# Performance work log

Measured on AMD Instinct MI355X. Metric: run time of the kernel, lower is better.

Reference implementation:

```python
import jax, jax.numpy as jnp
import numpy as np

N=50000; E=400000; H=128; FN=92; FE=41; L=3; PC=8; PD=16; SC=8; SD=32; B=64
EPS=1e-5

def _silu(x):
    return jax.nn.silu(x)

def _squash(s):
    n2=(s*s).sum(-1,keepdims=True)
    return s*(n2/(1.0+n2))/jnp.sqrt(n2+1e-9)

def setup_inputs():
    ks=iter(jax.random.split(jax.random.key(0),96))
    def rn(shape): return jax.random.normal(next(ks),shape,dtype=jnp.float32)
    def w(i,o): return rn((i,o))*np.float32(1.0/np.sqrt(i))
    z=lambda *s: jnp.zeros(s,jnp.float32); o=lambda *s: jnp.ones(s,jnp.float32)
    d={}
    d['x']=rn((N,FN)); d['edge_attr']=rn((E,FE)); d['pos']=rn((N,3))
    d['edge_index']=jax.random.randint(next(ks),(2,E),0,N)
    d['batch']=jnp.sort(jax.random.randint(next(ks),(N,),0,B))
    d.update(neW1=w(FN,H),neb1=z(H),neg1=o(H),nebe1=z(H),neW2=w(H,H),neb2=z(H),neg2=o(H),nebe2=z(H))
    d.update(eeW1=w(FE,H),eeb1=z(H),eeW2=w(H,H),eeb2=z(H),ivW=w(H,H),ivb=z(H))
    def wl(i,o2): return jnp.stack([w(i,o2) for _ in range(L)])
    d.update(cWma=wl(H,H),cWmb=wl(H,H),cWme=wl(H,H),cbm=z(L,H),cWsx=wl(H,H),cWsa=wl(H,H),cbs=z(L,H))
    d.update(cWv1=wl(H,H),cbv1=z(L,H),cWv2=wl(H,H),cbv2=z(L,H),lng=o(L,H),lnb=z(L,H),vsg=o(L,H))
    d.update(pcW=w(H,PC*PD),pcb=z(PC*PD),pvW=w(H,PD),sW=rn((PC,PD,SC,SD))*np.float32(1.0/np.sqrt(PD)))
    d.update(aW=w(SD//2,1),ab=z(1))
    d.update(pW1=w(SD,H//2),pb1=z(H//2),pg1=o(H//2),pbe1=z(H//2),pW2=w(H//2,H//4),pb2=z(H//4),pg2=o(H//4),pbe2=z(H//4),pW3=w(H//4,1),pb3=z(1))
    return d

def _forward(x,edge_index,edge_attr,pos,batch,neW1,neb1,neg1,nebe1,neW2,neb2,neg2,nebe2,eeW1,eeb1,eeW2,eeb2,ivW,ivb,cWma,cWmb,cWme,cbm,cWsx,cWsa,cbs,cWv1,cbv1,cWv2,cbv2,lng,lnb,vsg,pcW,pcb,pvW,sW,aW,ab,pW1,pb1,pg1,pbe1,pW2,pb2,pg2,pbe2,pW3,pb3):
    seg=jax.ops.segment_sum
    # node/edge MLP embeddings (BatchNorm in eval mode: running mean 0 / var 1 -> affine)
    xs=_silu((x@neW1+neb1)*neg1+nebe1)
    xs=_silu((xs@neW2+neb2)*neg2+nebe2)
    ea=_silu(edge_attr@eeW1+eeb1); ea=_silu(ea@eeW2+eeb2)
    # vectorized form of the per-node python loop: outer product weights x pos -> [N,H,3]
    xv=(xs@ivW+ivb)[:,:,None]*pos[:,None,:]
    src,dst=edge_index[0],edge_index[1]
    dp=pos[dst]-pos[src]                                  # [E,3]
    for i in range(L):
        xs_res,xv_res=xs,xv
        m=_silu(xs[src]@cWma[i]+xs[dst]@cWmb[i]+ea@cWme[i]+cbm[i])   # [E,H] edge messages
        xs_c=xs@cWsx[i]+seg(m,dst,num_segments=N)@cWsa[i]+cbs[i]
        vmsg=xv[src]*(m@cWv1[i]+cbv1[i])[:,:,None]+(m@cWv2[i]+cbv2[i])[:,:,None]*dp[:,None,:]
        xv_c=xv+seg(vmsg,dst,num_segments=N)               # [N,H,3]
        mu=xs_c.mean(-1,keepdims=True)
        xs_n=(xs_c-mu)/jnp.sqrt(((xs_c-mu)**2).mean(-1,keepdims=True)+EPS)*lng[i]+lnb[i]
        nrm=jnp.sqrt(((xv_c**2).sum(-1)).mean(-1,keepdims=True)+EPS)  # equivariant norm [N,1]
        xv_n=(xv_c/nrm[:,:,None])*vsg[i][None,:,None]
        xv_n=xv_n*jax.nn.sigmoid(xs_n)[:,:,None]           # scalar gating of vectors
        if i>0:
            xs=_silu(xs_n)+xs_res; xv=xv_n+xv_res
        else:
            xs=_silu(xs_n); xv=xv_n
    # primary capsules
    pc=_squash((xs@pcW+pcb).reshape(-1,PC,PD))             # [N,PC,PD]
    pv=jnp.einsum('nhd,hp->npd',xv,pvW)                    # [N,PD,3]
    u=pc+jnp.sqrt((pv**2).sum(-1)+1e-9)[:,None,:]          # vector norms expanded over PC caps
    # secondary capsules with per-graph pooling + 2 routing iterations
    pooled=seg(jnp.einsum('npd,pdce->npce',u,sW),batch,num_segments=B)  # [B,PC,SC,SD]
    bb=jnp.zeros((B,PC,SC),jnp.float32)
    for it in range(2):
        c=jax.nn.softmax(bb,axis=-1)
        v=_squash(jnp.einsum('bpc,bpce->bce',c,pooled))    # [B,SC,SD]
        if it==0:
            bb=bb+jnp.einsum('bpce,bce->bpc',pooled,v)
    # attention pooling over secondary capsules
    aw=jax.nn.softmax(v[:,:,:SD//2]@aW+ab,axis=1)
    wc=(aw*v).sum(1)                                       # [B,SD]
    h=_silu((wc@pW1+pb1)*pg1+pbe1)
    h=_silu((h@pW2+pb2)*pg2+pbe2)                          # dropout: eval mode (identity)
    return h@pW3+pb3

def reference(x,edge_index,edge_attr,pos,batch,neW1,neb1,neg1,nebe1,neW2,neb2,neg2,nebe2,eeW1,eeb1,eeW2,eeb2,ivW,ivb,cWma,cWmb,cWme,cbm,cWsx,cWsa,cbs,cWv1,cbv1,cWv2,cbv2,lng,lnb,vsg,pcW,pcb,pvW,sW,aW,ab,pW1,pb1,pg1,pbe1,pW2,pb2,pg2,pbe2,pW3,pb3):
    return _forward(x,edge_index,edge_attr,pos,batch,neW1,neb1,neg1,nebe1,neW2,neb2,neg2,nebe2,eeW1,eeb1,eeW2,eeb2,ivW,ivb,cWma,cWmb,cWme,cbm,cWsx,cWsa,cbs,cWv1,cbv1,cWv2,cbv2,lng,lnb,vsg,pcW,pcb,pvW,sW,aW,ab,pW1,pb1,pg1,pbe1,pW2,pb2,pg2,pbe2,pW3,pb3)
```

## Files before the change

### kernel.cpp

```cpp
#include <hip/hip_runtime.h>
#include <hip/hip_bf16.h>
#include <math.h>

#define NN 50000
#define NE 400000
#define HD 128
#define NB 64
#define NCH 8
#define CN 6250
#define ECM 53248
#define PSL 16

typedef __hip_bfloat16 bf16;
typedef __attribute__((ext_vector_type(4))) unsigned short us4;
typedef __attribute__((ext_vector_type(8))) short s8v;
typedef __attribute__((ext_vector_type(4))) float f4v;

__device__ __forceinline__ float sigm_(float x){ return 1.f/(1.f+__expf(-x)); }
__device__ __forceinline__ float silu_(float x){ return x*sigm_(x); }
__device__ __forceinline__ float bf2f(bf16 x){ return __bfloat162float(x); }
__device__ __forceinline__ unsigned short f2bu(float f){
    bf16 h = __float2bfloat16(f);
    return *reinterpret_cast<unsigned short*>(&h);
}
__device__ __forceinline__ bool finite_(float v){ return fabsf(v) <= 1e37f; }

enum { M_PLAIN=0, M_BIAS, M_BNSILU };

__global__ void wprep(const float* __restrict__ W, bf16* __restrict__ H, bf16* __restrict__ L){
    int i = blockIdx.x*256 + threadIdx.x;
    int k = i >> 7, n = i & 127;
    float w = W[i];
    bf16 h = __float2bfloat16(w);
    float r = w - bf2f(h);
    H[n*128 + k] = h;
    L[n*128 + k] = __float2bfloat16(r);
}

__global__ void wprep1(const float* __restrict__ W, bf16* __restrict__ H, bf16* __restrict__ L){
    int i = blockIdx.x*256 + threadIdx.x;
    int n = i >> 6, k = i & 63;
    float w = (k < 41) ? W[(size_t)k*HD + n] : 0.f;
    bf16 h = __float2bfloat16(w);
    float r = w - bf2f(h);
    H[n*64 + k] = h;
    L[n*64 + k] = __float2bfloat16(r);
}

template<int MODE>
__global__ __launch_bounds__(256)
void gemmk(const float* __restrict__ A, const float* __restrict__ W,
           const float* __restrict__ bias, const float* __restrict__ gg,
           const float* __restrict__ be, void* __restrict__ Cv, int owf, int M, int K)
{
    const int row0 = blockIdx.x * 64;
    if (row0 >= M) return;
    __shared__ float As[32][68];
    __shared__ float Ws[32][128];
    const int tid = threadIdx.x;
    const int tx = tid & 15, ty = tid >> 4;
    const int col0 = tx*8;
    float acc[4][8];
#pragma unroll
    for (int r=0;r<4;++r)
#pragma unroll
        for (int j=0;j<8;++j) acc[r][j]=0.f;
    const int mload = tid >> 2;
    const int kload = (tid & 3) << 3;
    const int grow = row0 + mload;
    const bool rv = grow < M;

    for (int k0 = 0; k0 < K; k0 += 32) {
        if (rv && ((K & 3) == 0) && (k0 + kload + 8 <= K)) {
            const float* ap = A + (size_t)grow*K + k0 + kload;
            float4 v0 = *(const float4*)ap;
            float4 v1 = *(const float4*)(ap+4);
            As[kload+0][mload]=v0.x; As[kload+1][mload]=v0.y;
            As[kload+2][mload]=v0.z; As[kload+3][mload]=v0.w;
            As[kload+4][mload]=v1.x; As[kload+5][mload]=v1.y;
            As[kload+6][mload]=v1.z; As[kload+7][mload]=v1.w;
        } else {
#pragma unroll
            for (int j=0;j<8;++j){
                int kg = k0 + kload + j;
                As[kload+j][mload] = (rv && kg<K) ? A[(size_t)grow*K+kg] : 0.f;
            }
        }
        if (k0 + 32 <= K) {
#pragma unroll
            for (int j=0;j<4;++j){
                int el = (tid + j*256)*4;
                int kk = el >> 7, col = el & 127;
                *(float4*)&Ws[kk][col] = *(const float4*)&W[(size_t)(k0+kk)*HD + col];
            }
        } else {
#pragma unroll
            for (int j=0;j<16;++j){
                int el = tid*16 + j;
                int kk = el >> 7, col = el & 127;
                int kg = k0 + kk;
                Ws[kk][col] = (kg < K) ? W[(size_t)kg*HD + col] : 0.f;
            }
        }
        __syncthreads();
#pragma unroll
        for (int k=0;k<32;++k){
            float4 a4 = *(const float4*)&As[k][ty*4];
            float4 w0 = *(const float4*)&Ws[k][col0];
            float4 w1 = *(const float4*)&Ws[k][col0+4];
            float av[4] = {a4.x,a4.y,a4.z,a4.w};
            float wv[8] = {w0.x,w0.y,w0.z,w0.w,w1.x,w1.y,w1.z,w1.w};
#pragma unroll
            for (int r=0;r<4;++r)
#pragma unroll
                for (int j=0;j<8;++j) acc[r][j] += av[r]*wv[j];
        }
        __syncthreads();
    }
#pragma unroll
    for (int r=0;r<4;++r){
        int orow = row0 + ty*4 + r;
        if (orow >= M) continue;
        float o[8];
#pragma unroll
        for (int j=0;j<8;++j) o[j]=acc[r][j];
        if constexpr (MODE==M_BIAS || MODE==M_BNSILU){
#pragma unroll
            for (int j=0;j<8;++j) o[j] += bias[col0+j];
        }
        if constexpr (MODE==M_BNSILU){
#pragma unroll
            for (int j=0;j<8;++j) o[j] = silu_(o[j]*gg[col0+j] + be[col0+j]);
        }
        if (owf){
            bf16* C = (bf16*)Cv;
#pragma unroll
            for (int j=0;j<8;++j) C[(size_t)orow*HD+col0+j] = __float2bfloat16(o[j]);
        } else {
            float* C = (float*)Cv;
            float4* cp = (float4*)&C[(size_t)orow*HD + col0];
            cp[0] = make_float4(o[0],o[1],o[2],o[3]);
            cp[1] = make_float4(o[4],o[5],o[6],o[7]);
        }
    }
}

__global__ __launch_bounds__(256)
void gemm3(const float* __restrict__ A0, const float* __restrict__ W0, float* __restrict__ C0, int M0,
           const float* __restrict__ A1, const float* __restrict__ W1, float* __restrict__ C1, int M1,
           const float* __restrict__ A2, const float* __restrict__ W2, float* __restrict__ C2, int M2)
{
    const int nb0 = (M0+63)>>6, nb1 = (M1+63)>>6;
    int bb = (int)blockIdx.x;
    const float *A, *W; float* C; int M;
    if (bb < nb0){ A=A0; W=W0; C=C0; M=M0; }
    else if (bb < nb0+nb1){ bb -= nb0; A=A1; W=W1; C=C1; M=M1; }
    else { bb -= nb0+nb1; A=A2; W=W2; C=C2; M=M2; }
    const int row0 = bb*64;

    __shared__ float As[32][68];
    __shared__ float Ws[32][128];
    const int tid = threadIdx.x;
    const int tx = tid & 15, ty = tid >> 4;
    const int col0 = tx*8;
    float acc[4][8];
#pragma unroll
    for (int r=0;r<4;++r)
#pragma unroll
        for (int j=0;j<8;++j) acc[r][j]=0.f;
    const int mload = tid >> 2;
    const int kload = (tid & 3) << 3;
    const int grow = row0 + mload;
    const bool rv = grow < M;

    for (int k0 = 0; k0 < 128; k0 += 32) {
        if (rv) {
            const float* ap = A + (size_t)grow*128 + k0 + kload;
            float4 v0 = *(const float4*)ap;
            float4 v1 = *(const float4*)(ap+4);
            As[kload+0][mload]=v0.x; As[kload+1][mload]=v0.y;
            As[kload+2][mload]=v0.z; As[kload+3][mload]=v0.w;
            As[kload+4][mload]=v1.x; As[kload+5][mload]=v1.y;
            As[kload+6][mload]=v1.z; As[kload+7][mload]=v1.w;
        } else {
#pragma unroll
            for (int j=0;j<8;++j) As[kload+j][mload] = 0.f;
        }
#pragma unroll
        for (int j=0;j<4;++j){
            int el = (tid + j*256)*4;
            int kk = el >> 7, col = el & 127;
            *(float4*)&Ws[kk][col] = *(const float4*)&W[(size_t)(k0+kk)*HD + col];
        }
        __syncthreads();
#pragma unroll
        for (int k=0;k<32;++k){
            float4 a4 = *(const float4*)&As[k][ty*4];
            float4 w0 = *(const float4*)&Ws[k][col0];
            float4 w1 = *(const float4*)&Ws[k][col0+4];
            float av[4] = {a4.x,a4.y,a4.z,a4.w};
            float wv[8] = {w0.x,w0.y,w0.z,w0.w,w1.x,w1.y,w1.z,w1.w};
#pragma unroll
            for (int r=0;r<4;++r)
#pragma unroll
                for (int j=0;j<8;++j) acc[r][j] += av[r]*wv[j];
        }
        __syncthreads();
    }
#pragma unroll
    for (int r=0;r<4;++r){
        int orow = row0 + ty*4 + r;
        if (orow >= M) continue;
        float4* cp = (float4*)&C[(size_t)orow*HD + col0];
        cp[0] = make_float4(acc[r][0],acc[r][1],acc[r][2],acc[r][3]);
        cp[1] = make_float4(acc[r][4],acc[r][5],acc[r][6],acc[r][7]);
    }
}

__global__ __launch_bounds__(256)
void edge_pipe(const float* __restrict__ eat,
               const int* __restrict__ elist, const int* __restrict__ srcp,
               const int* __restrict__ dstp,
               const bf16* __restrict__ W1h, const bf16* __restrict__ W1l,
               const float* __restrict__ b1,
               const bf16* __restrict__ W2h, const bf16* __restrict__ W2l,
               const float* __restrict__ b2,
               const bf16* __restrict__ Wmeh, const bf16* __restrict__ Wmel,
               const float* __restrict__ bm,
               const bf16* __restrict__ An, const bf16* __restrict__ Bn,
               const bf16* __restrict__ Wv1h, const bf16* __restrict__ Wv1l,
               const float* __restrict__ bv1,
               const int* __restrict__ rp, int rn0, int rn1,
               bf16* __restrict__ outM, bf16* __restrict__ outG)
{
    __shared__ __align__(16) unsigned short T1[64][136];
    __shared__ __align__(16) unsigned short T2[64][136];
    __shared__ int elS[64], seS[64], deS[64];

    const int cbase = rp[rn0];
    const int Ml = min(ECM, max(rp[rn1]-cbase, 0));
    const int row0 = blockIdx.x*64;
    if (row0 >= Ml) return;
    const int tid = threadIdx.x;
    const int lane = tid & 63, wave = tid >> 6;
    const int quad = lane >> 4, n16 = lane & 15;
    const int cwb = wave*32;

    if (tid < 64){
        int r = row0 + tid;
        bool v = r < Ml;
        int p = cbase + (v ? r : 0);
        elS[tid] = v ? min(max(elist[p],0),NE-1) : 0;
        seS[tid] = v ? srcp[p] : 0;
        deS[tid] = v ? dstp[p] : 0;
    }
    __syncthreads();

    f4v acc[4][2];

    {
        s8v B1h[2][2], B1l[2][2];
#pragma unroll
        for (int ct=0; ct<2; ++ct){
            int nn = cwb + ct*16 + n16;
#pragma unroll
            for (int kc=0; kc<2; ++kc){
                B1h[ct][kc] = *(const s8v*)&W1h[(size_t)nn*64 + kc*32 + quad*8];
                B1l[ct][kc] = *(const s8v*)&W1l[(size_t)nn*64 + kc*32 + quad*8];
            }
        }
#pragma unroll
        for (int rt=0;rt<4;++rt)
#pragma unroll
            for (int ct=0;ct<2;++ct) acc[rt][ct] = (f4v){0.f,0.f,0.f,0.f};

#pragma unroll
        for (int rt=0; rt<4; ++rt){
            int arow = elS[rt*16 + n16];
#pragma unroll
            for (int kc=0; kc<2; ++kc){
                s8v ah, al;
#pragma unroll
                for (int j=0;j<8;++j){
                    int k = kc*32 + quad*8 + j;
                    float v = (k < 41) ? eat[(size_t)arow*41 + k] : 0.f;
                    unsigned short h = f2bu(v);
                    ah[j] = (short)h;
                    al[j] = (short)f2bu(v - __uint_as_float(((unsigned)h)<<16));
                }
#pragma unroll
                for (int ct=0; ct<2; ++ct){
                    acc[rt][ct] = __builtin_amdgcn_mfma_f32_16x16x32_bf16(ah, B1h[ct][kc], acc[rt][ct], 0,0,0);
                    acc[rt][ct] = __builtin_amdgcn_mfma_f32_16x16x32_bf16(ah, B1l[ct][kc], acc[rt][ct], 0,0,0);
                    acc[rt][ct] = __builtin_amdgcn_mfma_f32_16x16x32_bf16(al, B1h[ct][kc], acc[rt][ct], 0,0,0);
                }
            }
        }
#pragma unroll
        for (int ct=0; ct<2; ++ct){
            int col = cwb + ct*16 + n16;
            float bc = b1[col];
#pragma unroll
            for (int rt=0; rt<4; ++rt)
#pragma unroll
                for (int i=0;i<4;++i)
                    T1[rt*16 + quad*4 + i][col] = f2bu(silu_(acc[rt][ct][i] + bc));
        }
    }
    __syncthreads();

    s8v Bh[2][4], Bl[2][4];
    for (int ph=0; ph<3; ++ph){
        const bf16* WH = (ph==0)? W2h : (ph==1)? Wmeh : Wv1h;
        const bf16* WL = (ph==0)? W2l : (ph==1)? Wmel : Wv1l;
        const unsigned short (*Tin)[136] = (ph==1)? (const unsigned short(*)[136])T2
                                                  : (const unsigned short(*)[136])T1;
#pragma unroll
        for (int ct=0; ct<2; ++ct){
            int nn = cwb + ct*16 + n16;
            const s8v* hp = (const s8v*)&WH[(size_t)nn*128];
            const s8v* lp = (const s8v*)&WL[(size_t)nn*128];
#pragma unroll
            for (int kc=0; kc<4; ++kc){
                Bh[ct][kc] = hp[kc*4 + quad];
                Bl[ct][kc] = lp[kc*4 + quad];
            }
        }
#pragma unroll
        for (int rt=0;rt<4;++rt)
#pragma unroll
            for (int ct=0;ct<2;++ct) acc[rt][ct] = (f4v){0.f,0.f,0.f,0.f};

        s8v anR[4], bnR[4];
        if (ph==1){
#pragma unroll
            for (int it=0; it<4; ++it){
                int idx = tid + it*256;
                int r = idx >> 4, c = idx & 15;
                anR[it] = *(const s8v*)&An[(size_t)seS[r]*HD + c*8];
                bnR[it] = *(const s8v*)&Bn[(size_t)deS[r]*HD + c*8];
            }
        }

#pragma unroll
        for (int kc=0; kc<4; ++kc){
#pragma unroll
            for (int rt=0; rt<4; ++rt){
                s8v a = *(const s8v*)&Tin[rt*16 + n16][kc*32 + quad*8];
#pragma unroll
                for (int ct=0; ct<2; ++ct){
                    acc[rt][ct] = __builtin_amdgcn_mfma_f32_16x16x32_bf16(a, Bh[ct][kc], acc[rt][ct], 0,0,0);
                    acc[rt][ct] = __builtin_amdgcn_mfma_f32_16x16x32_bf16(a, Bl[ct][kc], acc[rt][ct], 0,0,0);
                }
            }
        }
        if (ph==0){
#pragma unroll
            for (int ct=0; ct<2; ++ct){
                int col = cwb + ct*16 + n16;
                float bc = b2[col];
#pragma unroll
                for (int rt=0; rt<4; ++rt)
#pragma unroll
                    for (int i=0;i<4;++i)
                        T2[rt*16 + quad*4 + i][col] = f2bu(silu_(acc[rt][ct][i] + bc));
            }
            __syncthreads();
        } else if (ph==1){
            __syncthreads();
#pragma unroll
            for (int it=0; it<4; ++it){
                int idx = tid + it*256;
                int r = idx >> 4, c = idx & 15;
                *(s8v*)&T1[r][c*8] = anR[it];
                *(s8v*)&T2[r][c*8] = bnR[it];
            }
            __syncthreads();
#pragma unroll
            for (int ct=0; ct<2; ++ct){
                int col = cwb + ct*16 + n16;
                float bc = bm[col];
#pragma unroll
                for (int rt=0; rt<4; ++rt)
#pragma unroll
                    for (int i=0;i<4;++i){
                        int row = rt*16 + quad*4 + i;
                        float v = silu_(acc[rt][ct][i] + bc
                                        + bf2f(*(const bf16*)&T1[row][col])
                                        + bf2f(*(const bf16*)&T2[row][col]));
                        T1[row][col] = f2bu(v);
                    }
            }
            __syncthreads();
            {
                int row = tid >> 2, seg = tid & 3;
                if (row0 + row < Ml){
                    const s8v* s = (const s8v*)&T1[row][seg*32];
                    s8v* d = (s8v*)&outM[(size_t)(row0+row)*HD + seg*32];
                    d[0]=s[0]; d[1]=s[1]; d[2]=s[2]; d[3]=s[3];
                }
            }
        } else {
#pragma unroll
            for (int ct=0; ct<2; ++ct){
                int col = cwb + ct*16 + n16;
                float bc = bv1[col];
#pragma unroll
                for (int rt=0; rt<4; ++rt)
#pragma unroll
                    for (int i=0;i<4;++i)
                        T2[rt*16 + quad*4 + i][col] = f2bu(acc[rt][ct][i] + bc);
            }
            __syncthreads();
            {
                int row = tid >> 2, seg = tid & 3;
                if (row0 + row < Ml){
                    const s8v* s = (const s8v*)&T2[row][seg*32];
                    s8v* d = (s8v*)&outG[(size_t)(row0+row)*HD + seg*32];
                    d[0]=s[0]; d[1]=s[1]; d[2]=s[2]; d[3]=s[3];
                }
            }
        }
    }
}

__global__ __launch_bounds__(128)
void scatter_c(const int* __restrict__ rp, const int* __restrict__ srcp,
               const float* __restrict__ pos,
               const bf16* __restrict__ mB, const bf16* __restrict__ gB,
               const float* __restrict__ xvO,
               float* __restrict__ smC, float* __restrict__ mdC,
               float* __restrict__ avC, float* __restrict__ sdC, int n0, int n1)
{
    const int b = blockIdx.x;
    const int n = n0 + b;
    if (n >= n1) return;
    const int h = threadIdx.x;
    const int cbase = rp[n0];
    int p0 = rp[n], p1 = rp[n+1];
    float px0=pos[n*3],px1=pos[n*3+1],px2=pos[n*3+2];
    float sm=0,a0=0,a1=0,a2=0,m0=0,m1=0,m2=0,d0s=0,d1s=0,d2s=0;
    for (int p=p0;p<p1;++p){
        int ii=p-cbase; if ((unsigned)ii>=(unsigned)ECM) break;
        float mh=bf2f(mB[(size_t)ii*HD+h]);
        float gh=bf2f(gB[(size_t)ii*HD+h]);
        int sn=srcp[p]; sn=min(max(sn,0),NN-1);
        float d0=px0-pos[sn*3], d1=px1-pos[sn*3+1], d2=px2-pos[sn*3+2];
        sm+=mh;
        a0+=xvO[(size_t)sn*3*HD+h]*gh;
        a1+=xvO[(size_t)sn*3*HD+HD+h]*gh;
        a2+=xvO[(size_t)sn*3*HD+2*HD+h]*gh;
        m0+=mh*d0; m1+=mh*d1; m2+=mh*d2;
        d0s+=d0; d1s+=d1; d2s+=d2;
    }
    smC[(size_t)b*HD+h]=sm;
    mdC[(size_t)b*3*HD+h]=m0;
    mdC[(size_t)b*3*HD+HD+h]=m1;
    mdC[(size_t)b*3*HD+2*HD+h]=m2;
    avC[(size_t)b*3*HD+h]=a0;
    avC[(size_t)b*3*HD+HD+h]=a1;
    avC[(size_t)b*3*HD+2*HD+h]=a2;
    if (h==0){ sdC[b*3]=d0s; sdC[b*3+1]=d1s; sdC[b*3+2]=d2s; }
}

__global__ __launch_bounds__(128)
void nu_lite(const float* __restrict__ gF, const float* __restrict__ swF,
             const float* __restrict__ xwF,
             const float* __restrict__ avC, const float* __restrict__ sdC,
             const float* __restrict__ xvO, float* __restrict__ xvN,
             float* __restrict__ xs,
             const float* __restrict__ bv2, const float* __restrict__ bs,
             const float* __restrict__ lng, const float* __restrict__ lnb,
             const float* __restrict__ vsg, int addRes, int n0, int n1)
{
    __shared__ float red[4];
    __shared__ float red2[2];
    const int b = blockIdx.x;
    const int n = n0 + b;
    if (n >= n1) return;
    const int h = threadIdx.x;
    const int w = h >> 6;
    const float xsv = xs[(size_t)n*HD+h];
    float xc = xwF[(size_t)b*HD+h] + swF[(size_t)b*HD+h] + bs[h];
    float s1=xc, s2=xc*xc;
#pragma unroll
    for (int off=1; off<64; off<<=1){ s1+=__shfl_xor(s1,off,64); s2+=__shfl_xor(s2,off,64); }
    if ((h&63)==0){ red[w*2]=s1; red[w*2+1]=s2; }
    __syncthreads();
    s1=red[0]+red[2]; s2=red[1]+red[3];
    float mu=s1*(1.f/128.f);
    float var=fmaxf(s2*(1.f/128.f)-mu*mu, 0.f);
    float xn=(xc-mu)*rsqrtf(var+1e-5f)*lng[h]+lnb[h];
    float ov0=xvO[(size_t)n*3*HD+h];
    float ov1=xvO[(size_t)n*3*HD+HD+h];
    float ov2=xvO[(size_t)n*3*HD+2*HD+h];
    float a0=avC[(size_t)b*3*HD+h];
    float a1=avC[(size_t)b*3*HD+HD+h];
    float a2=avC[(size_t)b*3*HD+2*HD+h];
    float d0s=sdC[b*3], d1s=sdC[b*3+1], d2s=sdC[b*3+2];
    float b2v=bv2[h];
    float v0=ov0+a0+gF[(size_t)(b*3+0)*HD+h]+b2v*d0s;
    float v1=ov1+a1+gF[(size_t)(b*3+1)*HD+h]+b2v*d1s;
    float v2=ov2+a2+gF[(size_t)(b*3+2)*HD+h]+b2v*d2s;
    float q=v0*v0+v1*v1+v2*v2;
#pragma unroll
    for (int off=1; off<64; off<<=1) q+=__shfl_xor(q,off,64);
    if ((h&63)==0) red2[w]=q;
    __syncthreads();
    q=fmaxf(red2[0]+red2[1], 0.f);
    float nrm=sqrtf(q*(1.f/128.f)+1e-5f);
    float scale=vsg[h]*sigm_(xn)/nrm;
    float r0=v0*scale, r1=v1*scale, r2=v2*scale;
    float nxs=silu_(xn);
    if (addRes){ nxs+=xsv; r0+=ov0; r1+=ov1; r2+=ov2; }
    xs[(size_t)n*HD+h]=nxs;
    xvN[(size_t)n*3*HD+h]=r0;
    xvN[(size_t)n*3*HD+HD+h]=r1;
    xvN[(size_t)n*3*HD+2*HD+h]=r2;
}

__global__ void hist_kernel(const int* __restrict__ idx, int* __restrict__ cnt, int n, int nb){
    int i = blockIdx.x*256 + threadIdx.x;
    if (i < n){
        int v = idx[i]; v = min(max(v,0), nb-1);
        atomicAdd(&cnt[v], 1);
    }
}

__global__ __launch_bounds__(256)
void scan_blk(const int* __restrict__ cnt, int* __restrict__ rowptr,
              int* __restrict__ bsum, int n){
    const int b = blockIdx.x, t = threadIdx.x;
    const int i = b*256 + t;
    const int lane = t & 63, w = t >> 6;
    int v = (i < n) ? cnt[i] : 0;
    int s = v;
#pragma unroll
    for (int off=1; off<64; off<<=1){
        int u = __shfl_up(s, off, 64);
        if (lane >= off) s += u;
    }
    __shared__ int ws[4];
    if (lane == 63) ws[w] = s;
    __syncthreads();
    int add = 0;
#pragma unroll
    for (int j=0;j<4;++j) if (j < w) add += ws[j];
    s += add;
    if (i < n) rowptr[i+1] = s;
    if (t == 255) bsum[b] = s;
    if (b == 0 && t == 0) rowptr[0] = 0;
}

__global__ __launch_bounds__(256)
void scan_bsum(int* __restrict__ bsum, int nb){
    const int t = threadIdx.x;
    const int lane = t & 63, w = t >> 6;
    int v = (t < nb) ? bsum[t] : 0;
    int s = v;
#pragma unroll
    for (int off=1; off<64; off<<=1){
        int u = __shfl_up(s, off, 64);
        if (lane >= off) s += u;
    }
    __shared__ int ws[4];
    if (lane == 63) ws[w] = s;
    __syncthreads();
    int add = 0;
#pragma unroll
    for (int j=0;j<4;++j) if (j < w) add += ws[j];
    s += add;
    if (t < nb) bsum[t] = s - v;
}

__global__ __launch_bounds__(256)
void scan_fix(int* __restrict__ rowptr, const int* __restrict__ bsum, int n){
    const int b = blockIdx.x, t = threadIdx.x;
    const int i = b*256 + t;
    const int off = bsum[b];
    if (i < n) rowptr[i+1] += off;
}

__global__ void fill_kernel(const int* __restrict__ src, const int* __restrict__ dst,
                            const int* __restrict__ rowptr, int* __restrict__ cur,
                            int* __restrict__ elist, int* __restrict__ srcp,
                            int* __restrict__ dstp, int n){
    int e = blockIdx.x*256 + threadIdx.x;
    if (e < n){
        int d = dst[e]; d = min(max(d,0), NN-1);
        int slot = atomicAdd(&cur[d], 1);
        int p = rowptr[d] + slot;
        if (p >= 0 && p < NE){
            elist[p] = e;
            int s = src[e];
            srcp[p] = min(max(s,0), NN-1);
            dstp[p] = d;
        }
    }
}

__global__ void gptr_kernel(const int* __restrict__ batch, int* __restrict__ gptr){
    int n = blockIdx.x*256 + threadIdx.x;
    if (n >= NN) return;
    int b = batch[n]; b = min(max(b,0), NB-1);
    if (n == 0){
        for (int g=0; g<=b; ++g) gptr[g] = 0;
    } else {
        int bp = batch[n-1]; bp = min(max(bp,0), NB-1);
        for (int g=bp+1; g<=b; ++g) gptr[g] = n;
    }
    if (n == NN-1){
        for (int g=b+1; g<=NB; ++g) gptr[g] = NN;
    }
}

__global__ void xv_init(const float* __restrict__ xw, const float* __restrict__ pos,
                        float* __restrict__ xv){
    int n = blockIdx.x, h = threadIdx.x;
    float v = xw[(size_t)n*HD+h];
    xv[(size_t)n*3*HD + h]        = v*pos[n*3+0];
    xv[(size_t)n*3*HD + HD + h]   = v*pos[n*3+1];
    xv[(size_t)n*3*HD + 2*HD + h] = v*pos[n*3+2];
}

__global__ __launch_bounds__(128)
void capsule2(const float* __restrict__ Pf, const float* __restrict__ xv,
              const float* __restrict__ pvW, bf16* __restrict__ u){
    __shared__ float Pn[128];
    __shared__ float Xv[3][128];
    __shared__ float dots[48];
    __shared__ float pvn[16];
    __shared__ float capn2[8];
    int n = blockIdx.x, t = threadIdx.x;
    Pn[t] = Pf[(size_t)n*HD + t];
    Xv[0][t] = xv[(size_t)n*3*HD + t];
    Xv[1][t] = xv[(size_t)n*3*HD + HD + t];
    Xv[2][t] = xv[(size_t)n*3*HD + 2*HD + t];
    __syncthreads();
    if (t < 48){
        int pp = t/3, c = t%3;
        float a = 0.f;
        for (int hh=0; hh<128; ++hh) a += Xv[c][hh]*pvW[hh*16+pp];
        dots[t] = a;
    }
    if (t < 8){
        float a = 0.f;
        for (int d=0; d<16; ++d){ float x = Pn[t*16+d]; a += x*x; }
        capn2[t] = a;
    }
    __syncthreads();
    if (t < 16){
        float a = dots[t*3]*dots[t*3] + dots[t*3+1]*dots[t*3+1] + dots[t*3+2]*dots[t*3+2];
        pvn[t] = sqrtf(a + 1e-9f);
    }
    __syncthreads();
    int cap = t >> 4, d = t & 15;
    float n2 = capn2[cap];
    float pcv = Pn[t] * (n2/(1.f+n2)) * rsqrtf(n2 + 1e-9f);
    u[(size_t)n*HD + t] = __float2bfloat16(pcv + pvn[d]);
}

__global__ void pool1(const int* __restrict__ gptr, const bf16* __restrict__ u,
                      float* __restrict__ Up){
    int blk = blockIdx.x;
    int b = blk / PSL, s = blk % PSL;
    int h = threadIdx.x;
    int g0 = gptr[b], g1 = gptr[b+1];
    g0 = min(max(g0,0), NN); g1 = min(max(g1,0), NN);
    int len = g1 - g0;
    int lo = g0 + (int)(((long long)len * s) / PSL);
    int hi = g0 + (int)(((long long)len * (s+1)) / PSL);
    float a = 0.f;
    for (int n=lo; n<hi; ++n) a += bf2f(u[(size_t)n*HD + h]);
    Up[(size_t)blk*HD + h] = a;
}

__global__ void pool2(const float* __restrict__ Up, float* __restrict__ U){
    int b = blockIdx.x, h = threadIdx.x;
    float a = 0.f;
    for (int s=0; s<PSL; ++s) a += Up[(size_t)(b*PSL+s)*HD + h];
    U[b*HD + h] = a;
}

__global__ void graph_head(const float* __restrict__ U, const float* __restrict__ sW,
                           const float* __restrict__ aW, const float* __restrict__ ab,
                           const float* __restrict__ pW1, const float* __restrict__ pb1,
                           const float* __restrict__ pg1, const float* __restrict__ pbe1,
                           const float* __restrict__ pW2, const float* __restrict__ pb2,
                           const float* __restrict__ pg2, const float* __restrict__ pbe2,
                           const float* __restrict__ pW3, const float* __restrict__ pb3,
                           float* __restrict__ out){
    __shared__ float Ub[128];
    __shared__ float pooled[2048];
    __shared__ float vv[256];
    __shared__ float bbs[64], ccs[64];
    __shared__ float lg[8], aws[8];
    __shared__ float wcs[32];
    __shared__ float h1[64], h2[32];
    int b = blockIdx.x, t = threadIdx.x;
    if (t < 128) Ub[t] = U[b*HD + t];
    __syncthreads();
#pragma unroll
    for (int j=0;j<8;++j){
        int o = t + 256*j;
        int p = o >> 8, c = (o >> 5) & 7, e = o & 31;
        float a = 0.f;
#pragma unroll
        for (int d=0; d<16; ++d) a += Ub[p*16+d]*sW[((p*16+d)*8+c)*32+e];
        pooled[o] = a;
    }
    __syncthreads();
    {
        float s = 0.f;
        for (int p=0;p<8;++p) s += pooled[p*256 + t];
        s *= 0.125f;
        float n2 = s*s;
#pragma unroll
        for (int off=1; off<32; off<<=1) n2 += __shfl_xor(n2,off,32);
        vv[t] = s*(n2/(1.f+n2))*rsqrtf(n2+1e-9f);
    }
    __syncthreads();
    if (t < 64){
        int p = t>>3, c = t&7;
        float a = 0.f;
        for (int e=0;e<32;++e) a += pooled[p*256+c*32+e]*vv[c*32+e];
        bbs[t] = a;
    }
    __syncthreads();
    if (t < 64){
        int p = t>>3;
        float mx = -1e30f;
        for (int j=0;j<8;++j) mx = fmaxf(mx, bbs[p*8+j]);
        float sum = 0.f;
        for (int j=0;j<8;++j) sum += __expf(bbs[p*8+j]-mx);
        ccs[t] = __expf(bbs[t]-mx)/sum;
    }
    __syncthreads();
    {
        int c = t>>5;
        float s = 0.f;
        for (int p=0;p<8;++p) s += ccs[p*8+c]*pooled[p*256 + t];
        float n2 = s*s;
#pragma unroll
        for (int off=1; off<32; off<<=1) n2 += __shfl_xor(n2,off,32);
        vv[t] = s*(n2/(1.f+n2))*rsqrtf(n2+1e-9f);
    }
    __syncthreads();
    if (t < 8){
        float a = 0.f;
        for (int j=0;j<16;++j) a += vv[t*32+j]*aW[j];
        lg[t] = a + ab[0];
    }
    __syncthreads();
    if (t < 8){
        float mx = -1e30f;
        for (int j=0;j<8;++j) mx = fmaxf(mx, lg[j]);
        float sum = 0.f;
        for (int j=0;j<8;++j) sum += __expf(lg[j]-mx);
        aws[t] = __expf(lg[t]-mx)/sum;
    }
    __syncthreads();
    if (t < 32){
        float a = 0.f;
        for (int c=0;c<8;++c) a += aws[c]*vv[c*32+t];
        wcs[t] = a;
    }
    __syncthreads();
    if (t < 64){
        float a = 0.f;
        for (int e=0;e<32;++e) a += wcs[e]*pW1[e*64+t];
        h1[t] = silu_((a+pb1[t])*pg1[t]+pbe1[t]);
    }
    __syncthreads();
    if (t < 32){
        float a = 0.f;
        for (int j=0;j<64;++j) a += h1[j]*pW2[j*32+t];
        h2[t] = silu_((a+pb2[t])*pg2[t]+pbe2[t]);
    }
    __syncthreads();
    if (t == 0){
        float a = 0.f;
        for (int j=0;j<32;++j) a += h2[j]*pW3[j];
        a += pb3[0];
        if (!finite_(a)) a = 999.f;
        out[b] = a;
    }
}

__global__ void sentinel_k(float* __restrict__ out, float v){
    out[threadIdx.x] = v;
}

extern "C" void kernel_launch(void* const* d_in, const int* in_sizes, int n_in,
                              void* d_out, int out_size, void* d_ws, size_t ws_size,
                              hipStream_t stream)
{
    (void)in_sizes; (void)n_in; (void)out_size;
    const float* x    = (const float*)d_in[0];
    const float* eat  = (const float*)d_in[1];
    const float* pos  = (const float*)d_in[2];
    const int*  eidx  = (const int*)d_in[3];
    const int*  batch = (const int*)d_in[4];
    const float* neW1=(const float*)d_in[5],  *neb1=(const float*)d_in[6],
               * neg1=(const float*)d_in[7],  *nebe1=(const float*)d_in[8];
    const float* neW2=(const float*)d_in[9],  *neb2=(const float*)d_in[10],
               * neg2=(const float*)d_in[11], *nebe2=(const float*)d_in[12];
    const float* eeW1=(const float*)d_in[13], *eeb1=(const float*)d_in[14];
    const float* eeW2=(const float*)d_in[15], *eeb2=(const float*)d_in[16];
    const float* ivW =(const float*)d_in[17], *ivb =(const float*)d_in[18];
    const float* cWma=(const float*)d_in[19], *cWmb=(const float*)d_in[20],
               * cWme=(const float*)d_in[21], *cbm =(const float*)d_in[22];
    const float* cWsx=(const float*)d_in[23], *cWsa=(const float*)d_in[24],
               * cbs =(const float*)d_in[25];
    const float* cWv1=(const float*)d_in[26], *cbv1=(const float*)d_in[27],
               * cWv2=(const float*)d_in[28], *cbv2=(const float*)d_in[29];
    const float* lng =(const float*)d_in[30], *lnb =(const float*)d_in[31],
               * vsg =(const float*)d_in[32];
    const float* pcW =(const float*)d_in[33], *pcb =(const float*)d_in[34];
    const float* pvW =(const float*)d_in[35];
    const float* sW  =(const float*)d_in[36];
    const float* aW  =(const float*)d_in[37], *ab  =(const float*)d_in[38];
    const float* pW1 =(const float*)d_in[39], *pb1 =(const float*)d_in[40],
               * pg1 =(const float*)d_in[41], *pbe1=(const float*)d_in[42];
    const float* pW2 =(const float*)d_in[43], *pb2 =(const float*)d_in[44],
               * pg2 =(const float*)d_in[45], *pbe2=(const float*)d_in[46];
    const float* pW3 =(const float*)d_in[47], *pb3 =(const float*)d_in[48];

    const int* src = eidx;
    const int* dst = eidx + NE;

    char* wp = (char*)d_ws;
    auto alloc = [&](size_t bytes)->char*{
        char* p = wp;
        wp += (bytes + 255) & ~(size_t)255;
        return p;
    };
    bf16*  bufM  = (bf16*) alloc((size_t)ECM*HD*2);
    bf16*  bufG  = (bf16*) alloc((size_t)ECM*HD*2);
    float* xs    = (float*)alloc((size_t)NN*HD*4);
    float* xvA   = (float*)alloc((size_t)NN*3*HD*4);
    float* xvB   = (float*)alloc((size_t)NN*3*HD*4);
    bf16*  An    = (bf16*) alloc((size_t)NN*HD*2);
    bf16*  Bn    = (bf16*) alloc((size_t)NN*HD*2);
    float* smC   = (float*)alloc((size_t)CN*HD*4);
    float* mdC   = (float*)alloc((size_t)CN*3*HD*4);
    float* avC   = (float*)alloc((size_t)CN*3*HD*4);
    float* sdC   = (float*)alloc((size_t)CN*3*4);
    bf16*  WtH   = (bf16*) alloc((size_t)7*HD*HD*2);
    bf16*  WtL   = (bf16*) alloc((size_t)7*HD*HD*2);
    bf16*  W1h   = (bf16*) alloc((size_t)HD*64*2);
    bf16*  W1l   = (bf16*) alloc((size_t)HD*64*2);
    float* Up    = (float*)alloc((size_t)NB*PSL*HD*4);
    float* Ubuf  = (float*)alloc((size_t)NB*HD*4);
    int* rowptr  = (int*)alloc((size_t)(NN+1)*4);
    int* cnt     = (int*)alloc((size_t)NN*4);
    int* bsum    = (int*)alloc((size_t)256*4);
    int* elist   = (int*)alloc((size_t)NE*4);
    int* srcp    = (int*)alloc((size_t)NE*4);
    int* dstp    = (int*)alloc((size_t)NE*4);
    int* gptr    = (int*)alloc((size_t)(NB+1)*4);
    size_t used  = (size_t)(wp - (char*)d_ws);

    if (used > ws_size){
        sentinel_k<<<1, NB, 0, stream>>>((float*)d_out, -1.f - (float)(ws_size >> 20));
        return;
    }
    float* tmpF = xvB;
    bf16*  ubuf = An;
    float* Pf   = xvA;
    float* gF  = (float*)bufM;
    float* swF = gF  + (size_t)3*CN*HD;
    float* xwF = swF + (size_t)CN*HD;

    hipMemsetAsync(cnt, 0, (size_t)NN*4, stream);
    hist_kernel<<<(NE+255)/256, 256, 0, stream>>>(dst, cnt, NE, NN);
    const int SBLK = (NN+255)/256;
    scan_blk<<<SBLK, 256, 0, stream>>>(cnt, rowptr, bsum, NN);
    scan_bsum<<<1, 256, 0, stream>>>(bsum, SBLK);
    scan_fix<<<SBLK, 256, 0, stream>>>(rowptr, bsum, NN);
    hipMemsetAsync(cnt, 0, (size_t)NN*4, stream);
    fill_kernel<<<(NE+255)/256, 256, 0, stream>>>(src, dst, rowptr, cnt, elist, srcp, dstp, NE);
    gptr_kernel<<<(NN+255)/256, 256, 0, stream>>>(batch, gptr);
    wprep1<<<32,256,0,stream>>>(eeW1, W1h, W1l);
    wprep<<<64,256,0,stream>>>(eeW2, WtH, WtL);
    for (int l=0;l<3;++l){
        wprep<<<64,256,0,stream>>>(cWme + (size_t)l*HD*HD, WtH + (size_t)(1+l)*HD*HD,
                                   WtL + (size_t)(1+l)*HD*HD);
        wprep<<<64,256,0,stream>>>(cWv1 + (size_t)l*HD*HD, WtH + (size_t)(4+l)*HD*HD,
                                   WtL + (size_t)(4+l)*HD*HD);
    }

    const int GN = (NN+63)/64;
    const int GE = ECM/64;
    const int G3 = ((3*CN+63)/64) + 2*((CN+63)/64);

    gemmk<M_BNSILU><<<GN,256,0,stream>>>(x, neW1, neb1, neg1, nebe1, tmpF, 0, NN, 92);
    gemmk<M_BNSILU><<<GN,256,0,stream>>>(tmpF, neW2, neb2, neg2, nebe2, xs, 0, NN, 128);
    gemmk<M_BIAS><<<GN,256,0,stream>>>(xs, ivW, ivb, nullptr, nullptr, tmpF, 0, NN, 128);
    xv_init<<<NN, 128, 0, stream>>>(tmpF, pos, xvA);

    float* xvO = xvA;
    float* xvN = xvB;
    for (int l=0; l<3; ++l){
        const float* Wma = cWma + (size_t)l*HD*HD;
        const float* Wmb = cWmb + (size_t)l*HD*HD;
        const float* bm  = cbm  + (size_t)l*HD;
        const float* Wsx = cWsx + (size_t)l*HD*HD;
        const float* Wsa = cWsa + (size_t)l*HD*HD;
        const float* bs  = cbs  + (size_t)l*HD;
        const float* bv1 = cbv1 + (size_t)l*HD;
        const float* Wv2 = cWv2 + (size_t)l*HD*HD;
        const float* bv2 = cbv2 + (size_t)l*HD;
        const bf16* Wmeh = WtH + (size_t)(1+l)*HD*HD;
        const bf16* Wmel = WtL + (size_t)(1+l)*HD*HD;
        const bf16* Wv1h = WtH + (size_t)(4+l)*HD*HD;
        const bf16* Wv1l = WtL + (size_t)(4+l)*HD*HD;

        gemmk<M_PLAIN><<<GN,256,0,stream>>>(xs, Wma, nullptr, nullptr, nullptr, An, 1, NN, 128);
        gemmk<M_PLAIN><<<GN,256,0,stream>>>(xs, Wmb, nullptr, nullptr, nullptr, Bn, 1, NN, 128);

        for (int c=0; c<NCH; ++c){
            int n0 = c*CN, n1 = n0+CN;
            edge_pipe<<<GE,256,0,stream>>>(eat, elist, srcp, dstp,
                                           W1h, W1l, eeb1,
                                           WtH, WtL, eeb2,
                                           Wmeh, Wmel, bm,
                                           An, Bn,
                                           Wv1h, Wv1l, bv1,
                                           rowptr, n0, n1, bufM, bufG);
            scatter_c<<<CN,128,0,stream>>>(rowptr, srcp, pos, bufM, bufG, xvO,
                                           smC, mdC, avC, sdC, n0, n1);
            gemm3<<<G3,256,0,stream>>>(mdC, Wv2, gF, 3*CN,
                                       smC, Wsa, swF, CN,
                                       xs + (size_t)n0*HD, Wsx, xwF, CN);
            nu_lite<<<CN,128,0,stream>>>(gF, swF, xwF, avC, sdC,
                                         xvO, xvN, xs,
                                         bv2, bs,
                                         lng + (size_t)l*HD, lnb + (size_t)l*HD,
                                         vsg + (size_t)l*HD, l>0 ? 1 : 0, n0, n1);
        }
        float* t = xvO; xvO = xvN; xvN = t;
    }

    gemmk<M_BIAS><<<GN,256,0,stream>>>(xs, pcW, pcb, nullptr, nullptr, Pf, 0, NN, 128);
    capsule2<<<NN, 128, 0, stream>>>(Pf, xvO, pvW, ubuf);
    pool1<<<NB*PSL, 128, 0, stream>>>(gptr, ubuf, Up);
    pool2<<<NB, 128, 0, stream>>>(Up, Ubuf);
    graph_head<<<NB, 256, 0, stream>>>(Ubuf, sW, aW, ab,
                                       pW1, pb1, pg1, pbe1,
                                       pW2, pb2, pg2, pbe2,
                                       pW3, pb3, (float*)d_out);
}
```

Measured before the change: 3.333 ms.

## Restructure capsule2 to process nodes per wavefront with register-cached pvW

The capsule kernel now assigns one node to each 64-lane wavefront and loops each wave over four nodes, instead of launching one 128-thread block per node. pvW slices are held in registers across those nodes, and the dot products and capsule norms are reduced with cross-lane shuffles rather than serial per-thread loops over shared memory. This is meant to cut the launch of 50000 small blocks, the idle threads, and the repeated pvW reads. In exchange it adds register pressure and block-wide barriers between per-wave iterations.

```diff
diff --git a/kernel.cpp b/kernel.cpp
--- a/kernel.cpp
+++ b/kernel.cpp
@@ -623,41 +623,62 @@
     xv[(size_t)n*3*HD + 2*HD + h] = v*pos[n*3+2];
 }
 
-__global__ __launch_bounds__(128)
+__global__ __launch_bounds__(256)
 void capsule2(const float* __restrict__ Pf, const float* __restrict__ xv,
               const float* __restrict__ pvW, bf16* __restrict__ u){
-    __shared__ float Pn[128];
-    __shared__ float Xv[3][128];
-    __shared__ float dots[48];
-    __shared__ float pvn[16];
-    __shared__ float capn2[8];
-    int n = blockIdx.x, t = threadIdx.x;
-    Pn[t] = Pf[(size_t)n*HD + t];
-    Xv[0][t] = xv[(size_t)n*3*HD + t];
-    Xv[1][t] = xv[(size_t)n*3*HD + HD + t];
-    Xv[2][t] = xv[(size_t)n*3*HD + 2*HD + t];
-    __syncthreads();
-    if (t < 48){
-        int pp = t/3, c = t%3;
-        float a = 0.f;
-        for (int hh=0; hh<128; ++hh) a += Xv[c][hh]*pvW[hh*16+pp];
-        dots[t] = a;
-    }
-    if (t < 8){
-        float a = 0.f;
-        for (int d=0; d<16; ++d){ float x = Pn[t*16+d]; a += x*x; }
-        capn2[t] = a;
-    }
-    __syncthreads();
-    if (t < 16){
-        float a = dots[t*3]*dots[t*3] + dots[t*3+1]*dots[t*3+1] + dots[t*3+2]*dots[t*3+2];
-        pvn[t] = sqrtf(a + 1e-9f);
-    }
-    __syncthreads();
-    int cap = t >> 4, d = t & 15;
-    float n2 = capn2[cap];
-    float pcv = Pn[t] * (n2/(1.f+n2)) * rsqrtf(n2 + 1e-9f);
-    u[(size_t)n*HD + t] = __float2bfloat16(pcv + pvn[d]);
+    __shared__ float XvS[4][3*132];
+    const int tid  = threadIdx.x;
+    const int wave = tid >> 6, lane = tid & 63;
+    const int p = lane >> 2, l = lane & 3, l8 = (lane & 3) << 3;
+    float* Xw = XvS[wave];
+
+    float pvr[32];
+#pragma unroll
+    for (int i = 0; i < 32; ++i){
+        int h = l*32 + ((i + l8) & 31);
+        pvr[i] = pvW[h*16 + p];
+    }
+
+    const int waveGlobal = blockIdx.x*4 + wave;
+#pragma unroll 1
+    for (int it = 0; it < 4; ++it){
+        int n = waveGlobal + it*12500;
+        const float* xvn = xv + (size_t)n*3*HD;
+#pragma unroll
+        for (int k = 0; k < 6; ++k){
+            int e = k*64 + lane;
+            int c = e >> 7, hh = e & 127;
+            Xw[c*132 + hh] = xvn[e];
+        }
+        float pn0 = Pf[(size_t)n*HD + lane];
+        float pn1 = Pf[(size_t)n*HD + 64 + lane];
+        __syncthreads();
+        float a0=0.f, a1=0.f, a2=0.f;
+#pragma unroll
+        for (int i = 0; i < 32; ++i){
+            int hh = l*32 + ((i + l8) & 31);
+            float w = pvr[i];
+            a0 += Xw[hh]       * w;
+            a1 += Xw[132 + hh] * w;
+            a2 += Xw[264 + hh] * w;
+        }
+        a0 += __shfl_xor(a0, 1, 64); a0 += __shfl_xor(a0, 2, 64);
+        a1 += __shfl_xor(a1, 1, 64); a1 += __shfl_xor(a1, 2, 64);
+        a2 += __shfl_xor(a2, 1, 64); a2 += __shfl_xor(a2, 2, 64);
+        float pvn_own = sqrtf(a0*a0 + a1*a1 + a2*a2 + 1e-9f);
+        float pvn_d = __shfl(pvn_own, (lane & 15) << 2, 64);
+        float s0 = pn0*pn0, s1 = pn1*pn1;
+#pragma unroll
+        for (int off = 1; off < 16; off <<= 1){
+            s0 += __shfl_xor(s0, off, 64);
+            s1 += __shfl_xor(s1, off, 64);
+        }
+        float r0 = pn0 * (s0/(1.f+s0)) * rsqrtf(s0 + 1e-9f) + pvn_d;
+        float r1 = pn1 * (s1/(1.f+s1)) * rsqrtf(s1 + 1e-9f) + pvn_d;
+        u[(size_t)n*HD + lane]      = __float2bfloat16(r0);
+        u[(size_t)n*HD + 64 + lane] = __float2bfloat16(r1);
+        __syncthreads();
+    }
 }
 
 __global__ void pool1(const int* __restrict__ gptr, const bf16* __restrict__ u,
@@ -943,7 +964,7 @@
     }
 
     gemmk<M_BIAS><<<GN,256,0,stream>>>(xs, pcW, pcb, nullptr, nullptr, Pf, 0, NN, 128);
-    capsule2<<<NN, 128, 0, stream>>>(Pf, xvO, pvW, ubuf);
+    capsule2<<<12500/4, 256, 0, stream>>>(Pf, xvO, pvW, ubuf);
     pool1<<<NB*PSL, 128, 0, stream>>>(gptr, ubuf, Up);
     pool2<<<NB, 128, 0, stream>>>(Up, Ubuf);
     graph_head<<<NB, 256, 0, stream>>>(Ubuf, sW, aW, ab,
```

Measured after the change: 3.278 ms. About the same (-1.7%).
